# Performance work log

Hardware: AMD Instinct MI355X
Metric: run time of the kernel (lower is better)

The kernel has to match this reference:

```python
import jax, jax.numpy as jnp
import numpy as np

DIM = 768
B, N = 8, 2048


def setup_inputs() -> dict:
    key = jax.random.key(0)
    k = jax.random.split(key, 8)
    s = 1.0 / np.sqrt(DIM)
    return {
        "x": jax.random.normal(k[0], (B, N, DIM), jnp.float32),
        "x2": jax.random.normal(k[1], (B, N, DIM), jnp.float32),
        "x3": jax.random.normal(k[2], (B, N, DIM), jnp.float32),
        "W1": jax.random.uniform(k[3], (DIM, DIM), jnp.float32, -s, s),
        "b1": jax.random.uniform(k[4], (DIM,), jnp.float32, -s, s),
        "W2": jax.random.uniform(k[5], (DIM, DIM), jnp.float32, -s, s),
        "b2": jax.random.uniform(k[6], (DIM,), jnp.float32, -s, s),
        "w": jnp.ones((1,), jnp.float32),
    }


def _cross_attention(x, x2, W, b):
    # key = softmax(x2.transpose(1,2), dim=1) -> softmax over feature axis, then [B, D, N]
    key = jnp.swapaxes(jax.nn.softmax(x2, axis=-1), 1, 2)  # [B, D, N]
    query = jax.nn.softmax(x2, axis=1)                      # [B, N, D], softmax over tokens
    context = jnp.einsum('bnd,bdm->bnm', x, key)            # [B, N, N]
    atten = jnp.einsum('bnm,bmd->bnd', context, query)      # [B, N, D]
    return atten @ W.T + b


def reference(x, x2, x3, W1, b1, W2, b2, w):
    a1 = _cross_attention(x, x2, W1, b1)
    a2 = _cross_attention(x, x3, W2, b2)
    f = jax.nn.sigmoid(w)  # scalar gate, broadcast
    atten = a1 * f + a2 * f
    return atten + x
```

## Files before the change

kernel.cpp:

```cpp
#include <hip/hip_runtime.h>

#define DIMD 768
#define NTOK 2048
#define NB   8

typedef __attribute__((ext_vector_type(8))) short bfrag8;
typedef __attribute__((ext_vector_type(4))) float accf4;

__device__ __forceinline__ unsigned short f2bf(float f) {
  unsigned u = __float_as_uint(f);
  return (unsigned short)((u + 0x7fffu + ((u >> 16) & 1u)) >> 16);
}

__device__ __forceinline__ void glds16(const void* g, void* l) {
  __builtin_amdgcn_global_load_lds(
      (const __attribute__((address_space(1))) void*)g,
      (__attribute__((address_space(3))) void*)l, 16, 0, 0);
}


__device__ __forceinline__ void packw_body(int blk, const float* __restrict__ W1,
                                           const float* __restrict__ W2,
                                           unsigned short* __restrict__ Wcat) {
  int gid = blk * 256 + threadIdx.x;
  int r = gid / 192, c4 = (gid % 192) * 4;
  float4 a = *(const float4*)(W1 + (size_t)r * DIMD + c4);
  float4 b = *(const float4*)(W2 + (size_t)r * DIMD + c4);
  union { unsigned short us[4]; uint2 u2; } ra, rb;
  ra.us[0] = f2bf(a.x); ra.us[1] = f2bf(a.y); ra.us[2] = f2bf(a.z); ra.us[3] = f2bf(a.w);
  rb.us[0] = f2bf(b.x); rb.us[1] = f2bf(b.y); rb.us[2] = f2bf(b.z); rb.us[3] = f2bf(b.w);
  *(uint2*)(Wcat + (size_t)r * 1536 + c4) = ra.u2;
  *(uint2*)(Wcat + (size_t)r * 1536 + 768 + c4) = rb.u2;
}

__device__ __forceinline__ void packx_body(int blk, const float* __restrict__ x,
                                           unsigned short* __restrict__ xb) {
  size_t gid = (size_t)blk * 256 + threadIdx.x;
  const float4* x4 = (const float4*)x;
  float4 v0 = x4[gid * 2], v1 = x4[gid * 2 + 1];
  union { unsigned short us[8]; uint4 u4; } r;
  r.us[0] = f2bf(v0.x); r.us[1] = f2bf(v0.y); r.us[2] = f2bf(v0.z); r.us[3] = f2bf(v0.w);
  r.us[4] = f2bf(v1.x); r.us[5] = f2bf(v1.y); r.us[6] = f2bf(v1.z); r.us[7] = f2bf(v1.w);
  ((uint4*)xb)[gid] = r.u4;
}

template <int TMD, int TND, int EPI>
__device__ __forceinline__ void gemm_body(
    unsigned short* As, unsigned short* Bs, int bid,
    const unsigned short* __restrict__ A, const unsigned short* __restrict__ B,
    void* __restrict__ Cout, int K, int lda, int ldb, int ldc, int ntx,
    long long sA, long long sB, long long sC,
    const float* __restrict__ wg, const float* __restrict__ b1v,
    const float* __restrict__ b2v, const float* __restrict__ xres) {
  constexpr int TM = 64 * TMD, TN = 64 * TND;
  constexpr int ASZ = TM * 64, BSZ = TN * 64;
  __shared__ float csi[64 * TND];
  __shared__ float csir[64 * TMD];
  const int t = threadIdx.x, w = t >> 6, lane = t & 63;
  const int bz = bid & 7;
  const int r = bid >> 3;
  const int by = r / ntx, bx = r - by * ntx;
  const int m0 = by * TM, n0 = bx * TN;
  const unsigned short* Ab = A + (size_t)bz * sA;
  const unsigned short* Bb = B + (size_t)bz * sB;
  const int srow = lane >> 3;
  const int scol = (((lane & 7) ^ (lane >> 3)) * 8);

  auto stage = [&](int buf, int k0) {
    unsigned short* Ad = As + buf * ASZ;
    unsigned short* Bd = Bs + buf * BSZ;
#pragma unroll
    for (int l = 0; l < 2 * TND; ++l) {
      int chunk = l * 4 + w;
      int row = chunk * 8 + srow;
      glds16(Bb + (size_t)(n0 + row) * ldb + k0 + scol,
             (char*)Bd + chunk * 1024 + lane * 16);
    }
#pragma unroll
    for (int l = 0; l < 2 * TMD; ++l) {
      int chunk = l * 4 + w;
      int row = chunk * 8 + srow;
      glds16(Ab + (size_t)(m0 + row) * lda + k0 + scol,
             (char*)Ad + chunk * 1024 + lane * 16);
    }
  };

  stage(0, 0);

  if (EPI == 2) {
    for (int c = t; c < TN; c += 256) csi[c] = b1v[(size_t)bz * DIMD + n0 + c];
    for (int c = t; c < TM; c += 256) csir[c] = b1v[(size_t)bz * DIMD + m0 + c];
  }

  accf4 zero = {0.f, 0.f, 0.f, 0.f};
  accf4 acc[2 * TMD][2 * TND];
#pragma unroll
  for (int i = 0; i < 2 * TMD; ++i)
#pragma unroll
    for (int j = 0; j < 2 * TND; ++j) acc[i][j] = zero;

  const int wm = (w & 1) * (32 * TMD), wn = (w >> 1) * (32 * TND);
  const int lm = lane & 15, qd = lane >> 4;
  const int lsw = (lm & 7) << 3;

  __syncthreads();

  const int nt = K / 64;
  int cur = 0;
#pragma unroll 2
  for (int tt = 0; tt < nt; ++tt) {
    if (tt + 1 < nt) stage(cur ^ 1, (tt + 1) * 64);
    const unsigned short* Ar = As + cur * ASZ;
    const unsigned short* Br = Bs + cur * BSZ;
#pragma unroll
    for (int kc = 0; kc < 2; ++kc) {
      bfrag8 av[2 * TMD], bv[2 * TND];
      const int kslot = (((kc << 2) | qd) << 3) ^ lsw;
#pragma unroll
      for (int i = 0; i < 2 * TMD; ++i)
        av[i] = *(const bfrag8*)(Ar + (wm + i * 16 + lm) * 64 + kslot);
#pragma unroll
      for (int j = 0; j < 2 * TND; ++j)
        bv[j] = *(const bfrag8*)(Br + (wn + j * 16 + lm) * 64 + kslot);
      __builtin_amdgcn_s_setprio(1);
#pragma unroll
      for (int i = 0; i < 2 * TMD; ++i)
#pragma unroll
        for (int j = 0; j < 2 * TND; ++j)
          acc[i][j] = __builtin_amdgcn_mfma_f32_16x16x32_bf16(av[i], bv[j], acc[i][j], 0, 0, 0);
      __builtin_amdgcn_s_setprio(0);
    }
    if (tt + 1 < nt) {
      asm volatile("s_waitcnt vmcnt(0)\n\ts_barrier" ::: "memory");
    }
    cur ^= 1;
  }

  if (EPI == 0) {
    unsigned short* Cb = (unsigned short*)Cout + (size_t)bz * sC;
#pragma unroll
    for (int i = 0; i < 2 * TMD; ++i)
#pragma unroll
      for (int j = 0; j < 2 * TND; ++j) {
        int col = n0 + wn + j * 16 + lm;
#pragma unroll
        for (int rr = 0; rr < 4; ++rr) {
          int row = m0 + wm + i * 16 + qd * 4 + rr;
          Cb[(size_t)row * ldc + col] = f2bf(acc[i][j][rr]);
        }
      }
  } else if (EPI == 1) {
    float gate = 1.f / (1.f + __expf(-wg[0]));
    float* Co = (float*)Cout + (size_t)bz * sC;
    const float* Xr = xres + (size_t)bz * sC;
#pragma unroll
    for (int j = 0; j < 2 * TND; ++j) {
      int col = n0 + wn + j * 16 + lm;
      float gb = gate * (b1v[col] + b2v[col]);
#pragma unroll
      for (int i = 0; i < 2 * TMD; ++i)
#pragma unroll
        for (int rr = 0; rr < 4; ++rr) {
          int row = m0 + wm + i * 16 + qd * 4 + rr;
          size_t idx = (size_t)row * ldc + col;
          Co[idx] = gate * acc[i][j][rr] + gb + Xr[idx];
        }
    }
  } else {
    unsigned short* Cb = (unsigned short*)Cout + (size_t)bz * sC;
#pragma unroll
    for (int j = 0; j < 2 * TND; ++j) {
      int lc = wn + j * 16 + lm;
      int col = n0 + lc;
      float ci = csi[lc];
#pragma unroll
      for (int i = 0; i < 2 * TMD; ++i)
#pragma unroll
        for (int rr = 0; rr < 4; ++rr) {
          int row = m0 + wm + i * 16 + qd * 4 + rr;
          Cb[(size_t)row * ldc + col] = f2bf(acc[i][j][rr] * ci);
        }
    }
    if (m0 != n0) {
      unsigned short* mir = As;
      __syncthreads();
#pragma unroll
      for (int i = 0; i < 2 * TMD; ++i) {
        int lr0 = wm + i * 16 + qd * 4;
#pragma unroll
        for (int j = 0; j < 2 * TND; ++j) {
          int lc = wn + j * 16 + lm;
          int sw = (lc & 7) << 4;
          union { unsigned short us[4]; uint2 u2; } p;
#pragma unroll
          for (int rr = 0; rr < 4; ++rr)
            p.us[rr] = f2bf(acc[i][j][rr] * csir[lr0 + rr]);
          *(uint2*)&mir[lc * 128 + ((lr0) ^ sw)] = p.u2;
        }
      }
      __syncthreads();
      int e = t >> 1;
#pragma unroll
      for (int k = 0; k < 8; ++k) {
        int d0 = (((t & 1) << 3) + k) << 3;
        uint4 v = *(const uint4*)&mir[e * 128 + (d0 ^ ((e & 7) << 4))];
        *(uint4*)&Cb[(size_t)(n0 + e) * ldc + m0 + d0] = v;
      }
    }
  }
}

__global__ __launch_bounds__(256) void rowcol_kernel(
    const float* __restrict__ x2, const float* __restrict__ x3,
    float* __restrict__ csp1, float* __restrict__ csp2,
    float* __restrict__ rsf,
    const float* __restrict__ W1, const float* __restrict__ W2,
    unsigned short* __restrict__ Wcat, int npw) {
  int blk = blockIdx.x;
  if (blk >= 1024) {
    if (blk < 1024 + npw) packw_body(blk - 1024, W1, W2, Wcat);
    return;
  }
  const int sel = blk >> 9, b = (blk >> 6) & 7, tile = blk & 63;
  const float* xin = sel ? x3 : x2;
  float* csp = sel ? csp2 : csp1;
  float* rso = rsf + (size_t)sel * NB * NTOK + (size_t)b * NTOK + tile * 32;
  const float* xb_ = xin + ((size_t)b * NTOK + tile * 32) * DIMD;
  const int t = threadIdx.x, w = t >> 6, lane = t & 63;
  __shared__ float cred[4][DIMD];

  const int d0 = lane * 12;
  float cs[12];
#pragma unroll
  for (int i = 0; i < 12; ++i) cs[i] = 0.f;

#pragma unroll
  for (int v = 0; v < 8; ++v) {
    int tok = w * 8 + v;
    const float* row = xb_ + (size_t)tok * DIMD + d0;
    float4 a = *(const float4*)(row);
    float4 c = *(const float4*)(row + 4);
    float4 d = *(const float4*)(row + 8);
    float e[12];
    e[0] = __expf(a.x); e[1] = __expf(a.y); e[2] = __expf(a.z); e[3] = __expf(a.w);
    e[4] = __expf(c.x); e[5] = __expf(c.y); e[6] = __expf(c.z); e[7] = __expf(c.w);
    e[8] = __expf(d.x); e[9] = __expf(d.y); e[10] = __expf(d.z); e[11] = __expf(d.w);
    float rp = 0.f;
#pragma unroll
    for (int i = 0; i < 12; ++i) { rp += e[i]; cs[i] += e[i]; }
#pragma unroll
    for (int off = 32; off; off >>= 1) rp += __shfl_xor(rp, off, 64);
    if (lane == 0) rso[tok] = sqrtf(1.0f / rp);
  }
#pragma unroll
  for (int i = 0; i < 12; ++i) cred[w][d0 + i] = cs[i];
  __syncthreads();
#pragma unroll
  for (int i = 0; i < 3; ++i) {
    int d = t * 3 + i;
    float s = cred[0][d] + cred[1][d] + cred[2][d] + cred[3][d];
    csp[((size_t)b * 64 + tile) * DIMD + d] = s;
  }
}

__global__ __launch_bounds__(256) void ft_kernel(
    const float* __restrict__ x2, const float* __restrict__ x3,
    const float* __restrict__ rsf,
    unsigned short* __restrict__ Ft1, unsigned short* __restrict__ Ft2,
    const float* __restrict__ csp1, const float* __restrict__ csp2,
    float* __restrict__ civ1, float* __restrict__ civ2) {
  const int blk = blockIdx.x;
  if (blk >= 2048) {
    int idx = (blk - 2048) * 256 + threadIdx.x;
    int sel = idx / 6144, rem = idx - sel * 6144;
    int b = rem / DIMD, d = rem - b * DIMD;
    const float* csp = sel ? csp2 : csp1;
    float s = 0.f;
    const float* p = csp + (size_t)b * 64 * DIMD + d;
#pragma unroll 8
    for (int q = 0; q < 64; ++q) s += p[(size_t)q * DIMD];
    (sel ? civ2 : civ1)[rem] = 1.0f / s;
    return;
  }
  __shared__ __align__(16) unsigned short etile[192 * 72];
  const int sel = blk >> 10, lb = blk & 1023;
  const int b = lb >> 7, rr = lb & 127, ntile = rr >> 2, dc = rr & 3;
  const float* xin = sel ? x3 : x2;
  unsigned short* Ft = sel ? Ft2 : Ft1;
  const float* rsv = rsf + (size_t)sel * NB * NTOK + (size_t)b * NTOK + ntile * 64;
  const int t = threadIdx.x;

  const int tok = t >> 2, q4 = t & 3;
  const float* row = xin + ((size_t)b * NTOK + ntile * 64 + tok) * DIMD + dc * 192 + q4 * 48;
  const float fsc = rsv[tok];
#pragma unroll
  for (int j = 0; j < 12; ++j) {
    float4 v = *(const float4*)(row + j * 4);
    int dl = q4 * 48 + j * 4;
    etile[(dl + 0) * 72 + tok] = f2bf(__expf(v.x) * fsc);
    etile[(dl + 1) * 72 + tok] = f2bf(__expf(v.y) * fsc);
    etile[(dl + 2) * 72 + tok] = f2bf(__expf(v.z) * fsc);
    etile[(dl + 3) * 72 + tok] = f2bf(__expf(v.w) * fsc);
  }
  __syncthreads();
#pragma unroll
  for (int k = 0; k < 6; ++k) {
    int dl = (t >> 3) + k * 32;
    int g = t & 7;
    uint4 e8 = *(const uint4*)(etile + dl * 72 + g * 8);
    *(uint4*)(Ft + ((size_t)b * DIMD + dc * 192 + dl) * NTOK + ntile * 64 + g * 8) = e8;
  }
}

template <int TMD, int TND, int EPI>
__global__ __launch_bounds__(256) void mfma_bt(
    const unsigned short* __restrict__ A, const unsigned short* __restrict__ B,
    void* __restrict__ Cout, int K, int lda, int ldb, int ldc, int ntx,
    long long sA, long long sB, long long sC,
    const float* __restrict__ wg, const float* __restrict__ b1v,
    const float* __restrict__ b2v, const float* __restrict__ xres) {
  __shared__ __align__(16) unsigned short As[2 * 64 * TMD * 64];
  __shared__ __align__(16) unsigned short Bs[2 * 64 * TND * 64];
  gemm_body<TMD, TND, EPI>(As, Bs, blockIdx.x, A, B, Cout, K, lda, ldb, ldc, ntx,
                           sA, sB, sC, wg, b1v, b2v, xres);
}

__global__ __launch_bounds__(256) void sgemm_s(
    const unsigned short* __restrict__ Ft1, const float* __restrict__ civ1,
    const unsigned short* __restrict__ Ft2, const float* __restrict__ civ2,
    unsigned short* __restrict__ Ca, unsigned short* __restrict__ Cb) {
  __shared__ __align__(16) unsigned short As[2 * 128 * 64];
  __shared__ __align__(16) unsigned short Bs[2 * 128 * 64];
  int bid = blockIdx.x;
  int bz = bid & 7, r = bid >> 3;
  bool second = r >= 21;
  int tri = second ? r - 21 : r;
  int by = 0;
  while ((by + 1) * (by + 2) / 2 <= tri) ++by;
  int bx = tri - by * (by + 1) / 2;
  const unsigned short* F = second ? Ft2 : Ft1;
  const float* civ = second ? civ2 : civ1;
  unsigned short* C = second ? Cb : Ca;
  int enc = ((by * 6 + bx) << 3) | bz;
  gemm_body<2, 2, 2>(As, Bs, enc, F, F, C, NTOK, NTOK, NTOK, 1536, 6,
                     768LL * NTOK, 768LL * NTOK, 768LL * 1536,
                     nullptr, civ, nullptr, nullptr);
}

__global__ __launch_bounds__(256) void s2_packx_kernel(
    const unsigned short* __restrict__ Wcat, const unsigned short* __restrict__ Scat,
    unsigned short* __restrict__ Bt, const float* __restrict__ x,
    unsigned short* __restrict__ xb) {
  __shared__ __align__(16) unsigned short As[2 * 128 * 64];
  __shared__ __align__(16) unsigned short Bs[2 * 128 * 64];
  int blk = blockIdx.x;
  if (blk < 288) {
    gemm_body<2, 2, 0>(As, Bs, blk, Wcat, Scat, Bt, 1536, 1536, 1536, 768, 6,
                       0LL, 768LL * 1536, 768LL * 768,
                       nullptr, nullptr, nullptr, nullptr);
  } else {
    packx_body(blk - 288, x, xb);
  }
}

extern "C" void kernel_launch(void* const* d_in, const int* in_sizes, int n_in,
                              void* d_out, int out_size, void* d_ws, size_t ws_size,
                              hipStream_t stream) {
  const float* x  = (const float*)d_in[0];
  const float* x2 = (const float*)d_in[1];
  const float* x3 = (const float*)d_in[2];
  const float* W1 = (const float*)d_in[3];
  const float* b1 = (const float*)d_in[4];
  const float* W2 = (const float*)d_in[5];
  const float* b2 = (const float*)d_in[6];
  const float* w  = (const float*)d_in[7];
  float* out = (float*)d_out;
  char* ws = (char*)d_ws;

  unsigned short* Ft1  = (unsigned short*)(ws + 0);
  unsigned short* Ft2  = (unsigned short*)(ws + 25165824);
  unsigned short* Scat = (unsigned short*)(ws + 50331648);
  unsigned short* Wcat = (unsigned short*)(ws + 69206016);
  float* csp1 = (float*)(ws + 71565312);
  float* csp2 = (float*)(ws + 73138176);
  float* rsf  = (float*)(ws + 74711040);
  float* civ1 = (float*)(ws + 74842112);
  float* civ2 = (float*)(ws + 74866688);
  unsigned short* Bt = (unsigned short*)(ws + 0);
  unsigned short* xb = (unsigned short*)(ws + 9437184);

  dim3 blk(256);

  rowcol_kernel<<<1600, blk, 0, stream>>>(x2, x3, csp1, csp2, rsf, W1, W2, Wcat, 576);
  ft_kernel<<<2096, blk, 0, stream>>>(x2, x3, rsf, Ft1, Ft2, csp1, csp2, civ1, civ2);
  sgemm_s<<<336, blk, 0, stream>>>(Ft1, civ1, Ft2, civ2, Scat, Scat + 768);
  s2_packx_kernel<<<6432, blk, 0, stream>>>(Wcat, Scat, Bt, x, xb);
  mfma_bt<2, 2, 1><<<768, blk, 0, stream>>>(xb, Bt, out, DIMD, DIMD, DIMD, DIMD, 6,
                                            (long long)NTOK * DIMD, 768LL * 768,
                                            (long long)NTOK * DIMD, w, b1, b2, x);
}
```

Before: 308.8 us.

## Halve GEMM K-tile to 32 and split x packing across two kernels

The shared GEMM body now stages K tiles of 32 instead of 64, which halves LDS per block (so more blocks can be resident per CU) but doubles the number of loop iterations and barriers. The swizzle pattern is adjusted to the narrower tile. Half of the x-to-bf16 packing blocks move into the sgemm_s launch so they run alongside the small 336-block Gram GEMM that underfills the GPU, and the rest stay in s2_packx. xb moves to its own workspace region so it does not alias Ft1 while sgemm_s is still reading it.

```diff
diff --git a/kernel.cpp b/kernel.cpp
--- a/kernel.cpp
+++ b/kernel.cpp
@@ -46,14 +46,14 @@
 
 template <int TMD, int TND, int EPI>
 __device__ __forceinline__ void gemm_body(
-    unsigned short* As, unsigned short* Bs, int bid,
+    unsigned short* smem, int bid,
     const unsigned short* __restrict__ A, const unsigned short* __restrict__ B,
     void* __restrict__ Cout, int K, int lda, int ldb, int ldc, int ntx,
     long long sA, long long sB, long long sC,
     const float* __restrict__ wg, const float* __restrict__ b1v,
     const float* __restrict__ b2v, const float* __restrict__ xres) {
   constexpr int TM = 64 * TMD, TN = 64 * TND;
-  constexpr int ASZ = TM * 64, BSZ = TN * 64;
+  constexpr int ASZ = TM * 32, BSZ = TN * 32;
   __shared__ float csi[64 * TND];
   __shared__ float csir[64 * TMD];
   const int t = threadIdx.x, w = t >> 6, lane = t & 63;
@@ -63,23 +63,23 @@
   const int m0 = by * TM, n0 = bx * TN;
   const unsigned short* Ab = A + (size_t)bz * sA;
   const unsigned short* Bb = B + (size_t)bz * sB;
-  const int srow = lane >> 3;
-  const int scol = (((lane & 7) ^ (lane >> 3)) * 8);
+  const int srow = lane >> 2;
+  const int scol = (((lane & 3) ^ ((lane >> 2) & 3)) * 8);
 
   auto stage = [&](int buf, int k0) {
-    unsigned short* Ad = As + buf * ASZ;
-    unsigned short* Bd = Bs + buf * BSZ;
-#pragma unroll
-    for (int l = 0; l < 2 * TND; ++l) {
+    unsigned short* Ad = smem + buf * ASZ;
+    unsigned short* Bd = smem + 2 * ASZ + buf * BSZ;
+#pragma unroll
+    for (int l = 0; l < TND; ++l) {
       int chunk = l * 4 + w;
-      int row = chunk * 8 + srow;
+      int row = chunk * 16 + srow;
       glds16(Bb + (size_t)(n0 + row) * ldb + k0 + scol,
              (char*)Bd + chunk * 1024 + lane * 16);
     }
 #pragma unroll
-    for (int l = 0; l < 2 * TMD; ++l) {
+    for (int l = 0; l < TMD; ++l) {
       int chunk = l * 4 + w;
-      int row = chunk * 8 + srow;
+      int row = chunk * 16 + srow;
       glds16(Ab + (size_t)(m0 + row) * lda + k0 + scol,
              (char*)Ad + chunk * 1024 + lane * 16);
     }
@@ -101,35 +101,31 @@
 
   const int wm = (w & 1) * (32 * TMD), wn = (w >> 1) * (32 * TND);
   const int lm = lane & 15, qd = lane >> 4;
-  const int lsw = (lm & 7) << 3;
+  const int rslot = (qd ^ (lm & 3)) << 3;
 
   __syncthreads();
 
-  const int nt = K / 64;
+  const int nt = K / 32;
   int cur = 0;
 #pragma unroll 2
   for (int tt = 0; tt < nt; ++tt) {
-    if (tt + 1 < nt) stage(cur ^ 1, (tt + 1) * 64);
-    const unsigned short* Ar = As + cur * ASZ;
-    const unsigned short* Br = Bs + cur * BSZ;
-#pragma unroll
-    for (int kc = 0; kc < 2; ++kc) {
-      bfrag8 av[2 * TMD], bv[2 * TND];
-      const int kslot = (((kc << 2) | qd) << 3) ^ lsw;
-#pragma unroll
-      for (int i = 0; i < 2 * TMD; ++i)
-        av[i] = *(const bfrag8*)(Ar + (wm + i * 16 + lm) * 64 + kslot);
+    if (tt + 1 < nt) stage(cur ^ 1, (tt + 1) * 32);
+    const unsigned short* Ar = smem + cur * ASZ;
+    const unsigned short* Br = smem + 2 * ASZ + cur * BSZ;
+    bfrag8 av[2 * TMD], bv[2 * TND];
+#pragma unroll
+    for (int i = 0; i < 2 * TMD; ++i)
+      av[i] = *(const bfrag8*)(Ar + (wm + i * 16 + lm) * 32 + rslot);
+#pragma unroll
+    for (int j = 0; j < 2 * TND; ++j)
+      bv[j] = *(const bfrag8*)(Br + (wn + j * 16 + lm) * 32 + rslot);
+    __builtin_amdgcn_s_setprio(1);
+#pragma unroll
+    for (int i = 0; i < 2 * TMD; ++i)
 #pragma unroll
       for (int j = 0; j < 2 * TND; ++j)
-        bv[j] = *(const bfrag8*)(Br + (wn + j * 16 + lm) * 64 + kslot);
-      __builtin_amdgcn_s_setprio(1);
-#pragma unroll
-      for (int i = 0; i < 2 * TMD; ++i)
-#pragma unroll
-        for (int j = 0; j < 2 * TND; ++j)
-          acc[i][j] = __builtin_amdgcn_mfma_f32_16x16x32_bf16(av[i], bv[j], acc[i][j], 0, 0, 0);
-      __builtin_amdgcn_s_setprio(0);
-    }
+        acc[i][j] = __builtin_amdgcn_mfma_f32_16x16x32_bf16(av[i], bv[j], acc[i][j], 0, 0, 0);
+    __builtin_amdgcn_s_setprio(0);
     if (tt + 1 < nt) {
       asm volatile("s_waitcnt vmcnt(0)\n\ts_barrier" ::: "memory");
     }
@@ -182,7 +178,7 @@
         }
     }
     if (m0 != n0) {
-      unsigned short* mir = As;
+      unsigned short* mir = smem;
       __syncthreads();
 #pragma unroll
       for (int i = 0; i < 2 * TMD; ++i) {
@@ -319,19 +315,22 @@
     long long sA, long long sB, long long sC,
     const float* __restrict__ wg, const float* __restrict__ b1v,
     const float* __restrict__ b2v, const float* __restrict__ xres) {
-  __shared__ __align__(16) unsigned short As[2 * 64 * TMD * 64];
-  __shared__ __align__(16) unsigned short Bs[2 * 64 * TND * 64];
-  gemm_body<TMD, TND, EPI>(As, Bs, blockIdx.x, A, B, Cout, K, lda, ldb, ldc, ntx,
+  __shared__ __align__(16) unsigned short smem[2 * (64 * TMD + 64 * TND) * 32];
+  gemm_body<TMD, TND, EPI>(smem, blockIdx.x, A, B, Cout, K, lda, ldb, ldc, ntx,
                            sA, sB, sC, wg, b1v, b2v, xres);
 }
 
 __global__ __launch_bounds__(256) void sgemm_s(
     const unsigned short* __restrict__ Ft1, const float* __restrict__ civ1,
     const unsigned short* __restrict__ Ft2, const float* __restrict__ civ2,
-    unsigned short* __restrict__ Ca, unsigned short* __restrict__ Cb) {
-  __shared__ __align__(16) unsigned short As[2 * 128 * 64];
-  __shared__ __align__(16) unsigned short Bs[2 * 128 * 64];
+    unsigned short* __restrict__ Ca, unsigned short* __restrict__ Cb,
+    const float* __restrict__ x, unsigned short* __restrict__ xb, int npx) {
+  __shared__ __align__(16) unsigned short smem[4 * 128 * 32];
   int bid = blockIdx.x;
+  if (bid >= 336) {
+    if (bid < 336 + npx) packx_body(bid - 336, x, xb);
+    return;
+  }
   int bz = bid & 7, r = bid >> 3;
   bool second = r >= 21;
   int tri = second ? r - 21 : r;
@@ -342,7 +341,7 @@
   const float* civ = second ? civ2 : civ1;
   unsigned short* C = second ? Cb : Ca;
   int enc = ((by * 6 + bx) << 3) | bz;
-  gemm_body<2, 2, 2>(As, Bs, enc, F, F, C, NTOK, NTOK, NTOK, 1536, 6,
+  gemm_body<2, 2, 2>(smem, enc, F, F, C, NTOK, NTOK, NTOK, 1536, 6,
                      768LL * NTOK, 768LL * NTOK, 768LL * 1536,
                      nullptr, civ, nullptr, nullptr);
 }
@@ -350,16 +349,15 @@
 __global__ __launch_bounds__(256) void s2_packx_kernel(
     const unsigned short* __restrict__ Wcat, const unsigned short* __restrict__ Scat,
     unsigned short* __restrict__ Bt, const float* __restrict__ x,
-    unsigned short* __restrict__ xb) {
-  __shared__ __align__(16) unsigned short As[2 * 128 * 64];
-  __shared__ __align__(16) unsigned short Bs[2 * 128 * 64];
+    unsigned short* __restrict__ xb, int pxoff, int npx) {
+  __shared__ __align__(16) unsigned short smem[4 * 128 * 32];
   int blk = blockIdx.x;
   if (blk < 288) {
-    gemm_body<2, 2, 0>(As, Bs, blk, Wcat, Scat, Bt, 1536, 1536, 1536, 768, 6,
+    gemm_body<2, 2, 0>(smem, blk, Wcat, Scat, Bt, 1536, 1536, 1536, 768, 6,
                        0LL, 768LL * 1536, 768LL * 768,
                        nullptr, nullptr, nullptr, nullptr);
-  } else {
-    packx_body(blk - 288, x, xb);
+  } else if (blk < 288 + npx) {
+    packx_body(blk - 288 + pxoff, x, xb);
   }
 }
 
@@ -386,15 +384,16 @@
   float* rsf  = (float*)(ws + 74711040);
   float* civ1 = (float*)(ws + 74842112);
   float* civ2 = (float*)(ws + 74866688);
+  unsigned short* xb = (unsigned short*)(ws + 74891264);
   unsigned short* Bt = (unsigned short*)(ws + 0);
-  unsigned short* xb = (unsigned short*)(ws + 9437184);
 
   dim3 blk(256);
 
   rowcol_kernel<<<1600, blk, 0, stream>>>(x2, x3, csp1, csp2, rsf, W1, W2, Wcat, 576);
   ft_kernel<<<2096, blk, 0, stream>>>(x2, x3, rsf, Ft1, Ft2, csp1, csp2, civ1, civ2);
-  sgemm_s<<<336, blk, 0, stream>>>(Ft1, civ1, Ft2, civ2, Scat, Scat + 768);
-  s2_packx_kernel<<<6432, blk, 0, stream>>>(Wcat, Scat, Bt, x, xb);
+  sgemm_s<<<3408, blk, 0, stream>>>(Ft1, civ1, Ft2, civ2, Scat, Scat + 768,
+                                    x, xb, 3072);
+  s2_packx_kernel<<<3360, blk, 0, stream>>>(Wcat, Scat, Bt, x, xb, 3072, 3072);
   mfma_bt<2, 2, 1><<<768, blk, 0, stream>>>(xb, Bt, out, DIMD, DIMD, DIMD, DIMD, 6,
                                             (long long)NTOK * DIMD, 768LL * 768,
                                             (long long)NTOK * DIMD, w, b1, b2, x);
```

New measurement: 333.2 us. 7.9% more time.
